# Kernel tuning notes

Hardware: AMD Instinct MI355X
Metric: run time of the kernel (lower is better)

The kernel has to match this reference:

```python
import jax, jax.numpy as jnp
from jax import lax
import numpy as np

BN_EPS = 1e-5  # nn.BatchNorm2d default eps (eval mode with running stats)


def setup_inputs() -> dict:
    key = jax.random.key(0)
    ks = jax.random.split(key, 6)
    B, C, O, H, W = 4, 64, 64, 128, 128
    x = jax.random.normal(ks[0], (B, C, H, W), jnp.float32)
    # conv_offset: 27 = 3 * deform_groups * kh * kw output channels, zero-bias.
    # Scaled small to mimic the near-zero init of ModulatedDeformConv2dPack.
    w_off = jax.random.normal(ks[1], (27, C, 3, 3), jnp.float32) * 0.05
    b_off = jnp.zeros((27,), jnp.float32)
    weight = jax.random.normal(ks[2], (O, C, 3, 3), jnp.float32) * (1.0 / np.sqrt(C * 9))
    bias = jax.random.normal(ks[3], (O,), jnp.float32) * 0.1
    gamma = jax.random.normal(ks[4], (O,), jnp.float32) * 0.1 + 1.0
    beta = jax.random.normal(ks[5], (O,), jnp.float32) * 0.1
    running_mean = jnp.zeros((O,), jnp.float32)
    running_var = jnp.ones((O,), jnp.float32)
    return {"x": x, "w_off": w_off, "b_off": b_off, "weight": weight, "bias": bias,
            "gamma": gamma, "beta": beta, "running_mean": running_mean, "running_var": running_var}


def _dcn_bn_relu(x, w_off, b_off, weight, bias, gamma, beta, running_mean, running_var):
    B, C, H, W = x.shape
    O = weight.shape[0]
    K = 9  # 3x3 kernel taps
    # --- offset/mask conv (regular 3x3, stride 1, pad 1) ---
    off = lax.conv_general_dilated(x, w_off, (1, 1), ((1, 1), (1, 1)),
                                   dimension_numbers=("NCHW", "OIHW", "NCHW"))
    off = off + b_off[None, :, None, None]
    o1, o2, m = jnp.split(off, 3, axis=1)  # each [B,9,H,W]
    # mmcv layout: cat(o1,o2) then interpreted as (tap, [y,x]) pairs
    offset = jnp.concatenate([o1, o2], axis=1).reshape(B, K, 2, H, W)
    mask = jax.nn.sigmoid(m)  # [B,K,H,W]
    # --- sampling grid: p = (h - pad + i*dil + dy, w - pad + j*dil + dx) ---
    ky = (jnp.repeat(jnp.arange(3), 3) - 1).astype(x.dtype)  # [K]
    kx = (jnp.tile(jnp.arange(3), 3) - 1).astype(x.dtype)
    py = jnp.arange(H, dtype=x.dtype)[None, None, :, None] + ky[None, :, None, None] + offset[:, :, 0]
    px = jnp.arange(W, dtype=x.dtype)[None, None, None, :] + kx[None, :, None, None] + offset[:, :, 1]
    y0 = jnp.floor(py); x0 = jnp.floor(px)
    dy = py - y0; dx = px - x0  # [B,K,H,W]
    y0i = y0.astype(jnp.int32); x0i = x0.astype(jnp.int32)

    def gather(yi, xi):
        # zero outside bounds (mmcv bilinear semantics)
        valid = (yi >= 0) & (yi < H) & (xi >= 0) & (xi < W)
        yc = jnp.clip(yi, 0, H - 1)
        xc = jnp.clip(xi, 0, W - 1)
        g = jax.vmap(lambda xb, yb, xb2: xb[:, yb, xb2])(x, yc, xc)  # [B,C,K,H,W]
        return g * valid[:, None].astype(x.dtype)

    w00 = ((1 - dy) * (1 - dx))[:, None]
    w01 = ((1 - dy) * dx)[:, None]
    w10 = (dy * (1 - dx))[:, None]
    w11 = (dy * dx)[:, None]
    samp = (gather(y0i, x0i) * w00 + gather(y0i, x0i + 1) * w01 +
            gather(y0i + 1, x0i) * w10 + gather(y0i + 1, x0i + 1) * w11)
    samp = samp * mask[:, None]  # modulation, [B,C,K,H,W]
    # conv accumulation over (channel, tap)
    out = jnp.einsum("ock,bckhw->bohw", weight.reshape(O, C, K), samp)
    out = out + bias[None, :, None, None]
    # --- BatchNorm2d (eval, running stats) + ReLU ---
    scale = gamma / jnp.sqrt(running_var + BN_EPS)
    out = (out - running_mean[None, :, None, None]) * scale[None, :, None, None] + beta[None, :, None, None]
    return jax.nn.relu(out)


def reference(x, w_off, b_off, weight, bias, gamma, beta, running_mean, running_var):
    return _dcn_bn_relu(x, w_off, b_off, weight, bias, gamma, beta, running_mean, running_var)
```

## Files before the change

### kernel.cpp

```cpp
#include <hip/hip_runtime.h>
#include <hip/hip_bf16.h>


#define HH 128
#define WW 128
#define KP2 200

typedef __attribute__((ext_vector_type(8))) short bf16x8;
typedef __attribute__((ext_vector_type(4))) float f32x4;

__device__ __forceinline__ unsigned short f2bf(float f) {
    union { __hip_bfloat16 b; unsigned short u; } cv;
    cv.b = __float2bfloat16(f);
    return cv.u;
}
__device__ __forceinline__ float bf2f(unsigned short u) {
    union { unsigned int i; float f; } cv;
    cv.i = ((unsigned int)u) << 16;
    return cv.f;
}

#define WBM_ELEMS 36864
#define WBO_ELEMS 18432
#define XT_OFF    55296

__global__ __launch_bounds__(256) void transpose_kernel(
    const float* __restrict__ x,
    const float* __restrict__ w_off,
    const float* __restrict__ wgt,
    unsigned short* __restrict__ ws)
{
    __shared__ float tile[64 * 65];
    const int tid = threadIdx.x;

    {
        int t = blockIdx.x * 256 + tid;
        if (t < WBM_ELEMS) {
            int j = t & 7, lane = (t >> 3) & 63, nt = (t >> 9) & 3, kb = t >> 11;
            int k = kb * 32 + ((lane >> 4) << 3) + j;
            int n = nt * 16 + (lane & 15);
            int tap = k >> 6, c = k & 63;
            ws[t] = f2bf(wgt[n * 576 + c * 9 + tap]);
        } else if (t < WBM_ELEMS + WBO_ELEMS) {
            int t2 = t - WBM_ELEMS;
            int j = t2 & 7, lane = (t2 >> 3) & 63, nt = (t2 >> 9) & 1, kb = t2 >> 10;
            int k = kb * 32 + ((lane >> 4) << 3) + j;
            int n = nt * 16 + (lane & 15);
            int tap = k >> 6, c = k & 63;
            ws[t] = (n < 27) ? f2bf(w_off[n * 576 + c * 9 + tap]) : (unsigned short)0;
        }
    }

    const int bb  = blockIdx.x >> 8;
    const int hw0 = (blockIdx.x & 255) << 6;
    const float* xb = x + ((size_t)bb << 20);
#pragma unroll
    for (int it = 0; it < 16; ++it) {
        int idx = it * 256 + tid;
        int c = idx >> 6, i = idx & 63;
        tile[c * 65 + i] = xb[(c << 14) + hw0 + i];
    }
    __syncthreads();
    unsigned int* xtb = (unsigned int*)(ws + XT_OFF) + ((size_t)bb << 19);
#pragma unroll
    for (int it = 0; it < 8; ++it) {
        int idx = it * 256 + tid;
        int i = idx >> 5, c2 = idx & 31;
        unsigned int lo = (unsigned int)f2bf(tile[(2 * c2) * 65 + i]);
        unsigned int hi = (unsigned int)f2bf(tile[(2 * c2 + 1) * 65 + i]);
        xtb[(size_t)(hw0 + i) * 32 + c2] = lo | (hi << 16);
    }
}

__global__ __launch_bounds__(64) void DeformConv_14568529068723_kernel(
    const float* __restrict__ b_off,
    const float* __restrict__ bias,
    const float* __restrict__ gamma,
    const float* __restrict__ beta,
    const float* __restrict__ rmean,
    const float* __restrict__ rvar,
    const unsigned short* __restrict__ ws,
    float* __restrict__ out)
{
    __shared__ __align__(16) unsigned short samp[32 * KP2];
    __shared__ float eL[4][9][32];
    __shared__ int   oL[2][9][32];
    __shared__ float sbuf[176];

    const int tid  = threadIdx.x;
    const int px16 = tid & 15;
    const int cg   = tid >> 4;
    const int c8   = tid & 7;
    const int pxq  = tid >> 3;

    {
        float sc = gamma[tid] * __frsqrt_rn(rvar[tid] + 1e-5f);
        sbuf[tid] = sc;
        sbuf[64 + tid] = (bias[tid] - rmean[tid]) * sc + beta[tid];
        if (tid < 27) sbuf[128 + tid] = b_off[tid];
    }

    const int p0   = blockIdx.x * 32;
    const int b    = p0 >> 14;
    const int rem0 = p0 & 16383;
    const int h    = rem0 >> 7;
    const int w0   = rem0 & 127;
    const unsigned short* xt = ws + XT_OFF + ((size_t)b << 20);

    const bf16x8* WbM = (const bf16x8*)ws;
    const bf16x8* WbO = (const bf16x8*)(ws + WBM_ELEMS);

    __syncthreads();

    f32x4 accO[2][2];
#pragma unroll
    for (int mt = 0; mt < 2; ++mt)
#pragma unroll
        for (int q = 0; q < 2; ++q) accO[mt][q] = (f32x4){0.f, 0.f, 0.f, 0.f};

    for (int chk = 0; chk < 3; ++chk) {
#pragma unroll
        for (int tl = 0; tl < 3; ++tl) {
            int tap = chk * 3 + tl;
            int ky = tap / 3 - 1, kx = tap % 3 - 1;
            int yy = h + ky;
            int yc = min(max(yy, 0), HH - 1);
            bool oky = (yy >= 0) & (yy < HH);
#pragma unroll
            for (int it = 0; it < 4; ++it) {
                int px = it * 8 + pxq;
                int xx = w0 + px + kx;
                bool ok = oky & (xx >= 0) & (xx < WW);
                int pos = yc * WW + min(max(xx, 0), WW - 1);
                uint4 v = *(const uint4*)(xt + pos * 64 + (c8 << 3));
                if (!ok) { v.x = 0u; v.y = 0u; v.z = 0u; v.w = 0u; }
                *(uint4*)&samp[px * KP2 + tl * 64 + (c8 << 3)] = v;
            }
        }
        __syncthreads();
#pragma unroll
        for (int st = 0; st < 6; ++st) {
            int kb = chk * 6 + st;
            bf16x8 b0 = WbO[(kb * 2 + 0) * 64 + tid];
            bf16x8 b1 = WbO[(kb * 2 + 1) * 64 + tid];
#pragma unroll
            for (int mt = 0; mt < 2; ++mt) {
                bf16x8 af = *(const bf16x8*)&samp[(mt * 16 + px16) * KP2 + st * 32 + (cg << 3)];
                accO[mt][0] = __builtin_amdgcn_mfma_f32_16x16x32_bf16(af, b0, accO[mt][0], 0, 0, 0);
                accO[mt][1] = __builtin_amdgcn_mfma_f32_16x16x32_bf16(af, b1, accO[mt][1], 0, 0, 0);
            }
        }
        __syncthreads();
    }
    float* offs = (float*)samp;
    {
        int n0 = tid & 15;
        int mB = cg * 4;
#pragma unroll
        for (int mt = 0; mt < 2; ++mt)
#pragma unroll
            for (int r = 0; r < 4; ++r) {
                int pxc = mt * 16 + mB + r;
                offs[n0 * 32 + pxc] = accO[mt][0][r] + sbuf[128 + n0];
                int n1 = 16 + n0;
                if (n1 < 27) {
                    float vv = accO[mt][1][r] + sbuf[128 + n1];
                    if (n1 >= 18) vv = 1.0f / (1.0f + __expf(-vv));
                    offs[n1 * 32 + pxc] = vv;
                }
            }
    }
    __syncthreads();

#pragma unroll
    for (int base = 0; base < 288; base += 64) {
        int idx = base + tid;
        if (idx < 288) {
            int px = idx & 31, tap = idx >> 5;
            float o1 = offs[(2 * tap) * 32 + px];
            float o2 = offs[(2 * tap + 1) * 32 + px];
            float m  = offs[(18 + tap) * 32 + px];
            float py  = (float)(h + tap / 3 - 1) + o1;
            float pxf = (float)(w0 + px + tap % 3 - 1) + o2;
            float y0f = floorf(py), x0f = floorf(pxf);
            float dy = py - y0f, dx = pxf - x0f;
            int y0 = (int)y0f, x0 = (int)x0f;
            int y1 = y0 + 1, x1 = x0 + 1;
            int yc0 = min(max(y0, 0), HH - 1), yc1 = min(max(y1, 0), HH - 1);
            int xc0 = min(max(x0, 0), WW - 1), xc1 = min(max(x1, 0), WW - 1);
            float vy0 = (y0 >= 0 && y0 < HH) ? 1.0f : 0.0f;
            float vy1 = (y1 >= 0 && y1 < HH) ? 1.0f : 0.0f;
            float vx0 = (x0 >= 0 && x0 < WW) ? 1.0f : 0.0f;
            float vx1 = (x1 >= 0 && x1 < WW) ? 1.0f : 0.0f;
            float c00 = (1.0f - dy) * (1.0f - dx) * m * vy0 * vx0;
            float c01 = (1.0f - dy) * dx * m * vy0 * vx1;
            float c10 = dy * (1.0f - dx) * m * vy1 * vx0;
            float c11 = dy * dx * m * vy1 * vx1;
            int bx = min(xc0, WW - 2);
            bool s0 = (xc0 != bx), s1 = (xc1 != bx);
            eL[0][tap][px] = (s0 ? 0.f : c00) + (s1 ? 0.f : c01);
            eL[1][tap][px] = (s0 ? c00 : 0.f) + (s1 ? c01 : 0.f);
            eL[2][tap][px] = (s0 ? 0.f : c10) + (s1 ? 0.f : c11);
            eL[3][tap][px] = (s0 ? c10 : 0.f) + (s1 ? c11 : 0.f);
            oL[0][tap][px] = (yc0 * WW + bx) * 64;
            oL[1][tap][px] = (yc1 * WW + bx) * 64;
        }
    }
    __syncthreads();

    f32x4 acc[2][4];
#pragma unroll
    for (int mt = 0; mt < 2; ++mt)
#pragma unroll
        for (int nt = 0; nt < 4; ++nt) acc[mt][nt] = (f32x4){0.f, 0.f, 0.f, 0.f};

    for (int chk = 0; chk < 3; ++chk) {
#pragma unroll
        for (int tl = 0; tl < 3; ++tl) {
            int tap = chk * 3 + tl;
#pragma unroll
            for (int it = 0; it < 4; ++it) {
                int px = it * 8 + pxq;
                int o0 = oL[0][tap][px], o1r = oL[1][tap][px];
                float e0 = eL[0][tap][px], e1 = eL[1][tap][px];
                float e2 = eL[2][tap][px], e3 = eL[3][tap][px];
                uint4 a0 = *(const uint4*)(xt + o0 + (c8 << 3));
                uint4 a1 = *(const uint4*)(xt + o0 + 64 + (c8 << 3));
                uint4 b0 = *(const uint4*)(xt + o1r + (c8 << 3));
                uint4 b1 = *(const uint4*)(xt + o1r + 64 + (c8 << 3));
                const unsigned int* pa0 = (const unsigned int*)&a0;
                const unsigned int* pa1 = (const unsigned int*)&a1;
                const unsigned int* pb0 = (const unsigned int*)&b0;
                const unsigned int* pb1 = (const unsigned int*)&b1;
                uint4 pk;
                unsigned int* pp = (unsigned int*)&pk;
#pragma unroll
                for (int q = 0; q < 4; ++q) {
                    float lo = e0 * bf2f((unsigned short)(pa0[q] & 0xffff))
                             + e1 * bf2f((unsigned short)(pa1[q] & 0xffff))
                             + e2 * bf2f((unsigned short)(pb0[q] & 0xffff))
                             + e3 * bf2f((unsigned short)(pb1[q] & 0xffff));
                    float hi = e0 * bf2f((unsigned short)(pa0[q] >> 16))
                             + e1 * bf2f((unsigned short)(pa1[q] >> 16))
                             + e2 * bf2f((unsigned short)(pb0[q] >> 16))
                             + e3 * bf2f((unsigned short)(pb1[q] >> 16));
                    pp[q] = (unsigned int)f2bf(lo) | ((unsigned int)f2bf(hi) << 16);
                }
                *(uint4*)&samp[px * KP2 + tl * 64 + (c8 << 3)] = pk;
            }
        }
        __syncthreads();
#pragma unroll
        for (int st = 0; st < 6; ++st) {
            int kb = chk * 6 + st;
#pragma unroll
            for (int nt = 0; nt < 4; ++nt) {
                bf16x8 bf = WbM[(kb * 4 + nt) * 64 + tid];
#pragma unroll
                for (int mt = 0; mt < 2; ++mt) {
                    bf16x8 af = *(const bf16x8*)&samp[(mt * 16 + px16) * KP2 + st * 32 + (cg << 3)];
                    acc[mt][nt] = __builtin_amdgcn_mfma_f32_16x16x32_bf16(af, bf, acc[mt][nt], 0, 0, 0);
                }
            }
        }
        __syncthreads();
    }

    float* dT = (float*)samp;
    {
        int n0 = tid & 15;
        int mB = cg * 4;
#pragma unroll
        for (int mt = 0; mt < 2; ++mt)
#pragma unroll
            for (int nt = 0; nt < 4; ++nt)
#pragma unroll
                for (int r = 0; r < 4; ++r)
                    dT[(nt * 16 + n0) * 33 + mt * 16 + mB + r] = acc[mt][nt][r];
    }
    __syncthreads();
    {
        int px = tid & 31;
        int oh = tid >> 5;
#pragma unroll
        for (int i = 0; i < 32; ++i) {
            int o = 2 * i + oh;
            float v = dT[o * 33 + px];
            v = fmaxf(fmaf(v, sbuf[o], sbuf[64 + o]), 0.0f);
            out[(((size_t)(b * 64 + o)) << 14) + rem0 + px] = v;
        }
    }
}

extern "C" void kernel_launch(void* const* d_in, const int* in_sizes, int n_in,
                              void* d_out, int out_size, void* d_ws, size_t ws_size,
                              hipStream_t stream) {
    (void)in_sizes; (void)n_in; (void)ws_size; (void)out_size;
    const float* x     = (const float*)d_in[0];
    const float* w_off = (const float*)d_in[1];
    const float* b_off = (const float*)d_in[2];
    const float* wgt   = (const float*)d_in[3];
    const float* bias  = (const float*)d_in[4];
    const float* gamma = (const float*)d_in[5];
    const float* beta  = (const float*)d_in[6];
    const float* rmean = (const float*)d_in[7];
    const float* rvar  = (const float*)d_in[8];
    unsigned short* wsB = (unsigned short*)d_ws;
    float* outp = (float*)d_out;

    transpose_kernel<<<dim3(1024), dim3(256), 0, stream>>>(x, w_off, wgt, wsB);
    DeformConv_14568529068723_kernel<<<dim3(2048), dim3(64), 0, stream>>>(
        b_off, bias, gamma, beta, rmean, rvar, wsB, outp);
}
```

Before: 126.6 us.

## Split each 32-pixel block across two wavefronts, one per 16-pixel M-tile

The main kernel moves from one 64-thread wavefront per block to two wavefronts. Each wave owns one 16-pixel MFMA row tile, halving its accumulators and MFMA count, and the sampling, bilinear-coefficient and output-store loops are re-partitioned over 128 threads. The aim is more wave-level parallelism and latency hiding per block, plus fewer registers per thread. In exchange, each wave now loads the full weight B-fragments itself, so weight traffic per pixel doubles and there are more threads per barrier.

```diff
diff --git a/kernel.cpp b/kernel.cpp
--- a/kernel.cpp
+++ b/kernel.cpp
@@ -72,7 +72,7 @@
     }
 }
 
-__global__ __launch_bounds__(64) void DeformConv_14568529068723_kernel(
+__global__ __launch_bounds__(128) void DeformConv_14568529068723_kernel(
     const float* __restrict__ b_off,
     const float* __restrict__ bias,
     const float* __restrict__ gamma,
@@ -88,12 +88,14 @@
     __shared__ float sbuf[176];
 
     const int tid  = threadIdx.x;
-    const int px16 = tid & 15;
-    const int cg   = tid >> 4;
+    const int wv   = tid >> 6;
+    const int lane = tid & 63;
+    const int px16 = lane & 15;
+    const int cg   = lane >> 4;
     const int c8   = tid & 7;
     const int pxq  = tid >> 3;
 
-    {
+    if (tid < 64) {
         float sc = gamma[tid] * __frsqrt_rn(rvar[tid] + 1e-5f);
         sbuf[tid] = sc;
         sbuf[64 + tid] = (bias[tid] - rmean[tid]) * sc + beta[tid];
@@ -112,11 +114,9 @@
 
     __syncthreads();
 
-    f32x4 accO[2][2];
-#pragma unroll
-    for (int mt = 0; mt < 2; ++mt)
-#pragma unroll
-        for (int q = 0; q < 2; ++q) accO[mt][q] = (f32x4){0.f, 0.f, 0.f, 0.f};
+    f32x4 accO[2];
+#pragma unroll
+    for (int q = 0; q < 2; ++q) accO[q] = (f32x4){0.f, 0.f, 0.f, 0.f};
 
     for (int chk = 0; chk < 3; ++chk) {
 #pragma unroll
@@ -127,8 +127,8 @@
             int yc = min(max(yy, 0), HH - 1);
             bool oky = (yy >= 0) & (yy < HH);
 #pragma unroll
-            for (int it = 0; it < 4; ++it) {
-                int px = it * 8 + pxq;
+            for (int it = 0; it < 2; ++it) {
+                int px = it * 16 + pxq;
                 int xx = w0 + px + kx;
                 bool ok = oky & (xx >= 0) & (xx < WW);
                 int pos = yc * WW + min(max(xx, 0), WW - 1);
@@ -141,39 +141,34 @@
 #pragma unroll
         for (int st = 0; st < 6; ++st) {
             int kb = chk * 6 + st;
-            bf16x8 b0 = WbO[(kb * 2 + 0) * 64 + tid];
-            bf16x8 b1 = WbO[(kb * 2 + 1) * 64 + tid];
-#pragma unroll
-            for (int mt = 0; mt < 2; ++mt) {
-                bf16x8 af = *(const bf16x8*)&samp[(mt * 16 + px16) * KP2 + st * 32 + (cg << 3)];
-                accO[mt][0] = __builtin_amdgcn_mfma_f32_16x16x32_bf16(af, b0, accO[mt][0], 0, 0, 0);
-                accO[mt][1] = __builtin_amdgcn_mfma_f32_16x16x32_bf16(af, b1, accO[mt][1], 0, 0, 0);
-            }
+            bf16x8 b0 = WbO[(kb * 2 + 0) * 64 + lane];
+            bf16x8 b1 = WbO[(kb * 2 + 1) * 64 + lane];
+            bf16x8 af = *(const bf16x8*)&samp[(wv * 16 + px16) * KP2 + st * 32 + (cg << 3)];
+            accO[0] = __builtin_amdgcn_mfma_f32_16x16x32_bf16(af, b0, accO[0], 0, 0, 0);
+            accO[1] = __builtin_amdgcn_mfma_f32_16x16x32_bf16(af, b1, accO[1], 0, 0, 0);
         }
         __syncthreads();
     }
     float* offs = (float*)samp;
     {
-        int n0 = tid & 15;
+        int n0 = lane & 15;
         int mB = cg * 4;
 #pragma unroll
-        for (int mt = 0; mt < 2; ++mt)
-#pragma unroll
-            for (int r = 0; r < 4; ++r) {
-                int pxc = mt * 16 + mB + r;
-                offs[n0 * 32 + pxc] = accO[mt][0][r] + sbuf[128 + n0];
-                int n1 = 16 + n0;
-                if (n1 < 27) {
-                    float vv = accO[mt][1][r] + sbuf[128 + n1];
-                    if (n1 >= 18) vv = 1.0f / (1.0f + __expf(-vv));
-                    offs[n1 * 32 + pxc] = vv;
-                }
+        for (int r = 0; r < 4; ++r) {
+            int pxc = wv * 16 + mB + r;
+            offs[n0 * 32 + pxc] = accO[0][r] + sbuf[128 + n0];
+            int n1 = 16 + n0;
+            if (n1 < 27) {
+                float vv = accO[1][r] + sbuf[128 + n1];
+                if (n1 >= 18) vv = 1.0f / (1.0f + __expf(-vv));
+                offs[n1 * 32 + pxc] = vv;
             }
-    }
-    __syncthreads();
-
-#pragma unroll
-    for (int base = 0; base < 288; base += 64) {
+        }
+    }
+    __syncthreads();
+
+#pragma unroll
+    for (int base = 0; base < 288; base += 128) {
         int idx = base + tid;
         if (idx < 288) {
             int px = idx & 31, tap = idx >> 5;
@@ -208,19 +203,17 @@
     }
     __syncthreads();
 
-    f32x4 acc[2][4];
-#pragma unroll
-    for (int mt = 0; mt < 2; ++mt)
-#pragma unroll
-        for (int nt = 0; nt < 4; ++nt) acc[mt][nt] = (f32x4){0.f, 0.f, 0.f, 0.f};
+    f32x4 acc[4];
+#pragma unroll
+    for (int nt = 0; nt < 4; ++nt) acc[nt] = (f32x4){0.f, 0.f, 0.f, 0.f};
 
     for (int chk = 0; chk < 3; ++chk) {
 #pragma unroll
         for (int tl = 0; tl < 3; ++tl) {
             int tap = chk * 3 + tl;
 #pragma unroll
-            for (int it = 0; it < 4; ++it) {
-                int px = it * 8 + pxq;
+            for (int it = 0; it < 2; ++it) {
+                int px = it * 16 + pxq;
                 int o0 = oL[0][tap][px], o1r = oL[1][tap][px];
                 float e0 = eL[0][tap][px], e1 = eL[1][tap][px];
                 float e2 = eL[2][tap][px], e3 = eL[3][tap][px];
@@ -253,14 +246,11 @@
 #pragma unroll
         for (int st = 0; st < 6; ++st) {
             int kb = chk * 6 + st;
+            bf16x8 af = *(const bf16x8*)&samp[(wv * 16 + px16) * KP2 + st * 32 + (cg << 3)];
 #pragma unroll
             for (int nt = 0; nt < 4; ++nt) {
-                bf16x8 bf = WbM[(kb * 4 + nt) * 64 + tid];
-#pragma unroll
-                for (int mt = 0; mt < 2; ++mt) {
-                    bf16x8 af = *(const bf16x8*)&samp[(mt * 16 + px16) * KP2 + st * 32 + (cg << 3)];
-                    acc[mt][nt] = __builtin_amdgcn_mfma_f32_16x16x32_bf16(af, bf, acc[mt][nt], 0, 0, 0);
-                }
+                bf16x8 bf = WbM[(kb * 4 + nt) * 64 + lane];
+                acc[nt] = __builtin_amdgcn_mfma_f32_16x16x32_bf16(af, bf, acc[nt], 0, 0, 0);
             }
         }
         __syncthreads();
@@ -268,23 +258,21 @@
 
     float* dT = (float*)samp;
     {
-        int n0 = tid & 15;
+        int n0 = lane & 15;
         int mB = cg * 4;
 #pragma unroll
-        for (int mt = 0; mt < 2; ++mt)
-#pragma unroll
-            for (int nt = 0; nt < 4; ++nt)
-#pragma unroll
-                for (int r = 0; r < 4; ++r)
-                    dT[(nt * 16 + n0) * 33 + mt * 16 + mB + r] = acc[mt][nt][r];
+        for (int nt = 0; nt < 4; ++nt)
+#pragma unroll
+            for (int r = 0; r < 4; ++r)
+                dT[(nt * 16 + n0) * 33 + wv * 16 + mB + r] = acc[nt][r];
     }
     __syncthreads();
     {
         int px = tid & 31;
         int oh = tid >> 5;
 #pragma unroll
-        for (int i = 0; i < 32; ++i) {
-            int o = 2 * i + oh;
+        for (int i = 0; i < 16; ++i) {
+            int o = 4 * i + oh;
             float v = dT[o * 33 + px];
             v = fmaxf(fmaf(v, sbuf[o], sbuf[64 + o]), 0.0f);
             out[(((size_t)(b * 64 + o)) << 14) + rem0 + px] = v;
@@ -309,6 +297,6 @@
     float* outp = (float*)d_out;
 
     transpose_kernel<<<dim3(1024), dim3(256), 0, stream>>>(x, w_off, wgt, wsB);
-    DeformConv_14568529068723_kernel<<<dim3(2048), dim3(64), 0, stream>>>(
+    DeformConv_14568529068723_kernel<<<dim3(2048), dim3(128), 0, stream>>>(
         b_off, bias, gamma, beta, rmean, rvar, wsB, outp);
 }
```

New measurement: 121.4 us. -4.1%, faster.
